# Kernel optimization log

Measured on AMD Instinct MI355X. Metric: run time of the kernel, lower is better.

## Reference

```python
import jax, jax.numpy as jnp
import numpy as np

P = 16; N_SIDE = 14; N_PATCH = 196
ENC_DIM = 1024; ENC_DEPTH = 2; ENC_HEADS = 16; ENC_DH = 64
DEC_DIM = 512; DEC_DEPTH = 1; DEC_HEADS = 8; DEC_DH = 64
NUM_MASKED = int(0.75 * N_PATCH)  # 147


def _ln(x, s, b):
    m = jnp.mean(x, axis=-1, keepdims=True)
    v = jnp.var(x, axis=-1, keepdims=True)
    return (x - m) * jax.lax.rsqrt(v + 1e-5) * s + b


def _mha(x, Wqkv, Wo, heads, dh):
    B, N, _ = x.shape
    q, k, v = jnp.split(x @ Wqkv, 3, axis=-1)
    rs = lambda t: t.reshape(B, N, heads, dh).transpose(0, 2, 1, 3)
    q, k, v = rs(q), rs(k), rs(v)
    scores = jnp.einsum('bhqd,bhkd->bhqk', q, k) / jnp.sqrt(jnp.float32(dh))
    att = jax.nn.softmax(scores, axis=-1)
    o = jnp.einsum('bhqk,bhkd->bhqd', att, v).transpose(0, 2, 1, 3).reshape(B, N, heads * dh)
    return o @ Wo


def _transformer(x, params, depth, heads, dh, lnfs, lnfb):
    (ln1s, ln1b, Wqkv, Wo, ln2s, ln2b, W1, b1, W2, b2) = params
    for i in range(depth):
        x = x + _mha(_ln(x, ln1s[i], ln1b[i]), Wqkv[i], Wo[i], heads, dh)
        h = jax.nn.gelu(_ln(x, ln2s[i], ln2b[i]) @ W1[i] + b1[i])
        x = x + h @ W2[i] + b2[i]
    return _ln(x, lnfs, lnfb)


def setup_inputs() -> dict:
    key = jax.random.key(0)
    ks = jax.random.split(key, 24)
    B = 64
    w = lambda k, s: (jax.random.normal(k, s, jnp.float32) * 0.02)
    E, IE = ENC_DIM, ENC_HEADS * ENC_DH
    D, ID = DEC_DIM, DEC_HEADS * DEC_DH
    d = {}
    d['images'] = jax.random.normal(ks[0], (B, 224, 224, 3), jnp.float32)
    d['rand'] = jax.random.uniform(ks[1], (B, N_PATCH), dtype=jnp.float32)
    d['patch_W'] = w(ks[2], (P * P * 3, E)); d['patch_b'] = jnp.zeros((E,), jnp.float32)
    d['pos_emb'] = w(ks[3], (N_PATCH, E))
    d['enc_ln1s'] = jnp.ones((ENC_DEPTH, E), jnp.float32); d['enc_ln1b'] = jnp.zeros((ENC_DEPTH, E), jnp.float32)
    d['enc_Wqkv'] = w(ks[4], (ENC_DEPTH, E, 3 * IE)); d['enc_Wo'] = w(ks[5], (ENC_DEPTH, IE, E))
    d['enc_ln2s'] = jnp.ones((ENC_DEPTH, E), jnp.float32); d['enc_ln2b'] = jnp.zeros((ENC_DEPTH, E), jnp.float32)
    d['enc_W1'] = w(ks[6], (ENC_DEPTH, E, 4 * E)); d['enc_b1'] = jnp.zeros((ENC_DEPTH, 4 * E), jnp.float32)
    d['enc_W2'] = w(ks[7], (ENC_DEPTH, 4 * E, E)); d['enc_b2'] = jnp.zeros((ENC_DEPTH, E), jnp.float32)
    d['enc_lnfs'] = jnp.ones((E,), jnp.float32); d['enc_lnfb'] = jnp.zeros((E,), jnp.float32)
    d['e2d_W'] = w(ks[8], (E, D)); d['e2d_b'] = jnp.zeros((D,), jnp.float32)
    d['mask_token'] = w(ks[9], (D,))
    d['dec_pos'] = w(ks[10], (N_PATCH, D))
    d['dec_ln1s'] = jnp.ones((DEC_DEPTH, D), jnp.float32); d['dec_ln1b'] = jnp.zeros((DEC_DEPTH, D), jnp.float32)
    d['dec_Wqkv'] = w(ks[11], (DEC_DEPTH, D, 3 * ID)); d['dec_Wo'] = w(ks[12], (DEC_DEPTH, ID, D))
    d['dec_ln2s'] = jnp.ones((DEC_DEPTH, D), jnp.float32); d['dec_ln2b'] = jnp.zeros((DEC_DEPTH, D), jnp.float32)
    d['dec_W1'] = w(ks[13], (DEC_DEPTH, D, 4 * D)); d['dec_b1'] = jnp.zeros((DEC_DEPTH, 4 * D), jnp.float32)
    d['dec_W2'] = w(ks[14], (DEC_DEPTH, 4 * D, D)); d['dec_b2'] = jnp.zeros((DEC_DEPTH, D), jnp.float32)
    d['dec_lnfs'] = jnp.ones((D,), jnp.float32); d['dec_lnfb'] = jnp.zeros((D,), jnp.float32)
    d['pix_W'] = w(ks[15], (D, E)); d['pix_b'] = jnp.zeros((E,), jnp.float32)  # pixel_dim == encoder_dim per source
    return d


def reference(images, rand, patch_W, patch_b, pos_emb,
              enc_ln1s, enc_ln1b, enc_Wqkv, enc_Wo, enc_ln2s, enc_ln2b,
              enc_W1, enc_b1, enc_W2, enc_b2, enc_lnfs, enc_lnfb,
              e2d_W, e2d_b, mask_token, dec_pos,
              dec_ln1s, dec_ln1b, dec_Wqkv, dec_Wo, dec_ln2s, dec_ln2b,
              dec_W1, dec_b1, dec_W2, dec_b2, dec_lnfs, dec_lnfb,
              pix_W, pix_b):
    B = images.shape[0]
    # patch embed: [B,224,224,3] -> [B,196,768] -> [B,196,1024]
    x = images.reshape(B, N_SIDE, P, N_SIDE, P, 3).transpose(0, 1, 3, 2, 4, 5).reshape(B, N_PATCH, P * P * 3)
    patches = x @ patch_W + patch_b
    tokens = patches + pos_emb
    # random masking via argsort of uniform noise
    order = jnp.argsort(rand, axis=-1)
    m_idx = order[:, :NUM_MASKED]        # [B,147]
    u_idx = order[:, NUM_MASKED:]        # [B,49]
    unmasked = jnp.take_along_axis(tokens, u_idx[:, :, None], axis=1)
    enc_params = (enc_ln1s, enc_ln1b, enc_Wqkv, enc_Wo, enc_ln2s, enc_ln2b, enc_W1, enc_b1, enc_W2, enc_b2)
    encoded = _transformer(unmasked, enc_params, ENC_DEPTH, ENC_HEADS, ENC_DH, enc_lnfs, enc_lnfb)
    dec_tok = encoded @ e2d_W + e2d_b + dec_pos[u_idx]
    mask_toks = mask_token + dec_pos[m_idx]
    bidx = jnp.arange(B)[:, None]
    all_tok = jnp.zeros((B, N_PATCH, DEC_DIM), dec_tok.dtype)
    all_tok = all_tok.at[bidx, u_idx].set(dec_tok)
    all_tok = all_tok.at[bidx, m_idx].set(mask_toks)
    dec_params = (dec_ln1s, dec_ln1b, dec_Wqkv, dec_Wo, dec_ln2s, dec_ln2b, dec_W1, dec_b1, dec_W2, dec_b2)
    decoded = _transformer(all_tok, dec_params, DEC_DEPTH, DEC_HEADS, DEC_DH, dec_lnfs, dec_lnfb)
    pred = jnp.take_along_axis(decoded, m_idx[:, :, None], axis=1) @ pix_W + pix_b
    target = jnp.take_along_axis(patches, m_idx[:, :, None], axis=1)
    return jnp.mean((pred - target) ** 2)
```

## Files before the change

kernel.cpp:

```cpp
#include <hip/hip_runtime.h>

typedef __attribute__((ext_vector_type(8))) __bf16 bf16x8;
typedef __attribute__((ext_vector_type(4))) float f32x4;

#define OFF_PATCH 0ull
#define OFF_X     25690112ull
#define OFF_LN    51380224ull
#define OFF_QKV   64225280ull
#define OFF_HID   103022592ull
#define OFF_WP    154402816ull
#define OFF_ORD   214695936ull
#define OFF_PART  214746112ull

#define WP_PATCH   0ull
#define WP_ENC_QKV 786432ull
#define WP_ENC_WO  7077888ull
#define WP_ENC_W1  9175040ull
#define WP_ENC_W2  17563648ull
#define WP_E2D     25952256ull
#define WP_DEC_QKV 26476544ull
#define WP_DEC_WO  27262976ull
#define WP_DEC_W1  27525120ull
#define WP_DEC_W2  28573696ull
#define WP_PIX     29622272ull

#define OM_BF16 0
#define OM_F32  1
#define OM_ACC  2
#define OM_GELU 3

__device__ __forceinline__ float b2f(unsigned short u) {
    return __uint_as_float(((unsigned int)u) << 16);
}
__device__ __forceinline__ unsigned short f2b(float f) {
    unsigned int x = __float_as_uint(f);
    x += 0x7fffu + ((x >> 16) & 1u);
    return (unsigned short)(x >> 16);
}
__device__ __forceinline__ float gelu_f(float x) {
    float u2 = 1.5957691216057308f * x * (1.f + 0.044715f * x * x);
    return x / (1.f + __expf(-u2));
}
__device__ __forceinline__ void gload16(const void* g, void* l) {
    __builtin_amdgcn_global_load_lds((const __attribute__((address_space(1))) void*)g,
                                     (__attribute__((address_space(3))) void*)l, 16, 0, 0);
}

__global__ __launch_bounds__(256) void pack_w(const float* __restrict__ in,
                                              unsigned short* __restrict__ out, int K, int N) {
    __shared__ float tile[32][33];
    int kt = blockIdx.y * 32, nt = blockIdx.x * 32;
    int tx = threadIdx.x & 31, ty = threadIdx.x >> 5;
#pragma unroll
    for (int i = 0; i < 32; i += 8) tile[ty + i][tx] = in[(size_t)(kt + ty + i) * N + nt + tx];
    __syncthreads();
#pragma unroll
    for (int i = 0; i < 32; i += 8)
        out[(size_t)(nt + ty + i) * K + kt + tx] = f2b(tile[tx][ty + i]);
}

__global__ __launch_bounds__(256) void patchify_kernel(const float* __restrict__ img,
                                                       unsigned short* __restrict__ Xp) {
    const long long total = 12544ll * 768;
    for (long long e = (long long)blockIdx.x * 256 + threadIdx.x; e < total;
         e += (long long)gridDim.x * 256) {
        int row = (int)(e / 768), k = (int)(e % 768);
        int b = row / 196, pi = row % 196;
        int py = pi / 14, px = pi % 14;
        int r = k / 48, rem = k % 48;
        int c = rem / 3, ch = rem % 3;
        long long src = (((long long)(b * 224 + py * 16 + r)) * 224 + (px * 16 + c)) * 3 + ch;
        Xp[e] = f2b(img[src]);
    }
}

template <int OM, bool ATOMIC>
__global__ __launch_bounds__(256) void gemm2(const unsigned short* __restrict__ A,
                                             const unsigned short* __restrict__ Bt,
                                             void* __restrict__ Cv,
                                             const float* __restrict__ bias,
                                             int M, int N, int K, int Kc) {
    __shared__ __align__(16) unsigned short As[2][128 * 64];
    __shared__ __align__(16) unsigned short Bs[2][128 * 64];
    const int tid = threadIdx.x, wave = tid >> 6, lane = tid & 63;
    int nwg = gridDim.x * gridDim.y;
    int orig = blockIdx.y * gridDim.x + blockIdx.x;
    int q = nwg >> 3, r8 = nwg & 7, xcd = orig & 7, off = orig >> 3;
    int wg = (xcd < r8 ? xcd * (q + 1) : r8 * (q + 1) + (xcd - r8) * q) + off;
    const int brow = (wg / gridDim.x) * 128, bcol = (wg % gridDim.x) * 128;
    const int kBeg = blockIdx.z * Kc;
    const int fr = lane & 15, fq = lane >> 4;
    const int wr = (wave >> 1) * 64, wc = (wave & 1) * 64;
    const int srow = wave * 32 + (lane >> 3);
    const int sca = ((lane & 7) ^ (lane >> 3)) * 8;
    const unsigned short* Ag = A + (size_t)(brow + srow) * K + kBeg + sca;
    const unsigned short* Bg = Bt + (size_t)(bcol + srow) * K + kBeg + sca;

    f32x4 acc[4][4];
#pragma unroll
    for (int m = 0; m < 4; ++m)
#pragma unroll
        for (int n = 0; n < 4; ++n) acc[m][n] = (f32x4){0.f, 0.f, 0.f, 0.f};

    auto stage = [&](int buf, int k0) {
        unsigned short* AsW = &As[buf][(wave * 32) * 64];
        unsigned short* BsW = &Bs[buf][(wave * 32) * 64];
#pragma unroll
        for (int i = 0; i < 4; ++i) {
            gload16(Ag + (size_t)(i * 8) * K + k0, AsW + i * 8 * 64);
            gload16(Bg + (size_t)(i * 8) * K + k0, BsW + i * 8 * 64);
        }
    };
    auto compute = [&](int buf) {
        const char* ab = (const char*)&As[buf][0];
        const char* bb = (const char*)&Bs[buf][0];
        const int sw = (fr & 7) << 4;
#pragma unroll
        for (int kk = 0; kk < 2; ++kk) {
            bf16x8 af[4], bf[4];
#pragma unroll
            for (int m = 0; m < 4; ++m)
                af[m] = *(const bf16x8*)(ab + (wr + m * 16 + fr) * 128 +
                                         ((kk * 64 + fq * 16) ^ sw));
#pragma unroll
            for (int n = 0; n < 4; ++n)
                bf[n] = *(const bf16x8*)(bb + (wc + n * 16 + fr) * 128 +
                                         ((kk * 64 + fq * 16) ^ sw));
#pragma unroll
            for (int m = 0; m < 4; ++m)
#pragma unroll
                for (int n = 0; n < 4; ++n)
                    acc[m][n] = __builtin_amdgcn_mfma_f32_16x16x32_bf16(af[m], bf[n],
                                                                       acc[m][n], 0, 0, 0);
        }
    };

    const int nt = Kc >> 6;
    stage(0, 0);
    __syncthreads();
    int cur = 0;
    for (int t = 0; t < nt - 1; ++t) {
        stage(cur ^ 1, (t + 1) << 6);
        compute(cur);
        __syncthreads();
        cur ^= 1;
    }
    compute(cur);

    const bool addBias = (bias != nullptr) && (kBeg == 0);
#pragma unroll
    for (int m = 0; m < 4; ++m) {
        int rb = brow + wr + m * 16 + fq * 4;
#pragma unroll
        for (int r = 0; r < 4; ++r) {
            int row = rb + r;
            if (row < M) {
#pragma unroll
                for (int n = 0; n < 4; ++n) {
                    int col = bcol + wc + n * 16 + fr;
                    float v = acc[m][n][r];
                    if (addBias) v += bias[col];
                    size_t o = (size_t)row * N + col;
                    if constexpr (ATOMIC) atomicAdd((float*)Cv + o, v);
                    else if constexpr (OM == OM_BF16) ((unsigned short*)Cv)[o] = f2b(v);
                    else if constexpr (OM == OM_F32) ((float*)Cv)[o] = v;
                    else if constexpr (OM == OM_ACC) ((float*)Cv)[o] += v;
                    else ((unsigned short*)Cv)[o] = f2b(gelu_f(v));
                }
            }
        }
    }
}

template <int N, int H, int NW>
__global__ __launch_bounds__(NW * 64) void attn_mfma(const unsigned short* __restrict__ qkv,
                                                     unsigned short* __restrict__ out) {
    constexpr int Npad = ((N + 31) / 32) * 32;
    constexpr int NT = Npad / 16;
    constexpr int KS = Npad / 32;
    constexpr int PS = Npad + 8;
    constexpr int SQ = 3 * H * 64, SO = H * 64;
    __shared__ __align__(16) unsigned short Kl[Npad * 64];
    __shared__ __align__(16) unsigned short Vt[64 * PS];
    __shared__ __align__(16) unsigned short Pl[NW * 16 * PS];
    const int b = blockIdx.x / H, h = blockIdx.x % H;
    const unsigned short* base = qkv + (size_t)b * N * SQ;
    const int qoff = h * 64, koff = (H + h) * 64, voff = (2 * H + h) * 64;
    const int tid = threadIdx.x, wave = tid >> 6, lane = tid & 63;
    const int fr = lane & 15, fq = lane >> 4;

    for (int idx = tid; idx < Npad * 8; idx += NW * 64) {
        int row = idx >> 3, ch = idx & 7;
        uint4 v = {0u, 0u, 0u, 0u};
        if (row < N) v = *(const uint4*)(base + (size_t)row * SQ + koff + ch * 8);
        *(uint4*)((char*)Kl + row * 128 + ((ch * 16) ^ ((row & 7) << 4))) = v;
    }
    for (int idx = tid; idx < Npad * 32; idx += NW * 64) {
        int key = idx >> 5, d2 = (idx & 31) * 2;
        unsigned int v = 0;
        if (key < N) v = *(const unsigned int*)(base + (size_t)key * SQ + voff + d2);
        Vt[d2 * PS + key] = (unsigned short)(v & 0xffffu);
        Vt[(d2 + 1) * PS + key] = (unsigned short)(v >> 16);
    }
    __syncthreads();

    unsigned short* pw = Pl + wave * 16 * PS;
    for (int qt = wave; qt < NT; qt += NW) {
        const int q0 = qt * 16;
        int qr = q0 + fr;
        if (qr > N - 1) qr = N - 1;
        const unsigned short* qp = base + (size_t)qr * SQ + qoff + fq * 8;
        bf16x8 aq0 = *(const bf16x8*)qp;
        bf16x8 aq1 = *(const bf16x8*)(qp + 32);
        f32x4 sa[NT];
#pragma unroll
        for (int ct = 0; ct < NT; ++ct) sa[ct] = (f32x4){0.f, 0.f, 0.f, 0.f};
#pragma unroll
        for (int ct = 0; ct < NT; ++ct) {
            const char* kb = (const char*)Kl + (ct * 16 + fr) * 128;
            bf16x8 kf0 = *(const bf16x8*)(kb + ((fq * 16) ^ ((fr & 7) << 4)));
            bf16x8 kf1 = *(const bf16x8*)(kb + ((64 + fq * 16) ^ ((fr & 7) << 4)));
            sa[ct] = __builtin_amdgcn_mfma_f32_16x16x32_bf16(aq0, kf0, sa[ct], 0, 0, 0);
            sa[ct] = __builtin_amdgcn_mfma_f32_16x16x32_bf16(aq1, kf1, sa[ct], 0, 0, 0);
        }
        float mrow[4] = {-3e38f, -3e38f, -3e38f, -3e38f};
#pragma unroll
        for (int ct = 0; ct < NT; ++ct) {
            bool ok = (ct * 16 + fr) < N;
#pragma unroll
            for (int r = 0; r < 4; ++r) {
                float s = ok ? sa[ct][r] * 0.125f : -3e38f;
                sa[ct][r] = s;
                mrow[r] = fmaxf(mrow[r], s);
            }
        }
#pragma unroll
        for (int off = 1; off <= 8; off <<= 1)
#pragma unroll
            for (int r = 0; r < 4; ++r) mrow[r] = fmaxf(mrow[r], __shfl_xor(mrow[r], off));
        float ssum[4] = {0.f, 0.f, 0.f, 0.f};
#pragma unroll
        for (int ct = 0; ct < NT; ++ct)
#pragma unroll
            for (int r = 0; r < 4; ++r) {
                float p = __expf(sa[ct][r] - mrow[r]);
                sa[ct][r] = p;
                ssum[r] += p;
            }
#pragma unroll
        for (int off = 1; off <= 8; off <<= 1)
#pragma unroll
            for (int r = 0; r < 4; ++r) ssum[r] += __shfl_xor(ssum[r], off);
#pragma unroll
        for (int ct = 0; ct < NT; ++ct)
#pragma unroll
            for (int r = 0; r < 4; ++r)
                pw[(fq * 4 + r) * PS + ct * 16 + fr] = f2b(sa[ct][r]);
        f32x4 oa[4];
#pragma unroll
        for (int vt = 0; vt < 4; ++vt) oa[vt] = (f32x4){0.f, 0.f, 0.f, 0.f};
#pragma unroll
        for (int ks = 0; ks < KS; ++ks) {
            bf16x8 pa = *(const bf16x8*)(pw + fr * PS + ks * 32 + fq * 8);
#pragma unroll
            for (int vt = 0; vt < 4; ++vt) {
                bf16x8 vf = *(const bf16x8*)(&Vt[(vt * 16 + fr) * PS + ks * 32 + fq * 8]);
                oa[vt] = __builtin_amdgcn_mfma_f32_16x16x32_bf16(pa, vf, oa[vt], 0, 0, 0);
            }
        }
        float inv[4];
#pragma unroll
        for (int r = 0; r < 4; ++r) inv[r] = 1.f / ssum[r];
#pragma unroll
        for (int vt = 0; vt < 4; ++vt)
#pragma unroll
            for (int r = 0; r < 4; ++r) {
                int q = q0 + fq * 4 + r;
                if (q < N)
                    out[((size_t)b * N + q) * SO + h * 64 + vt * 16 + fr] =
                        f2b(oa[vt][r] * inv[r]);
            }
    }
}

__global__ __launch_bounds__(256) void argsort_kernel(const float* __restrict__ rnd,
                                                      int* __restrict__ ord) {
    __shared__ float vals[196];
    int b = blockIdx.x, t = threadIdx.x;
    if (t < 196) vals[t] = rnd[b * 196 + t];
    __syncthreads();
    if (t < 196) {
        float v = vals[t];
        int rank = 0;
        for (int j = 0; j < 196; ++j) {
            float vj = vals[j];
            rank += (vj < v) || (vj == v && j < t);
        }
        ord[b * 196 + rank] = t;
    }
}

__global__ __launch_bounds__(256) void gather_unmasked(const unsigned short* __restrict__ patches,
                                                       const float* __restrict__ pos,
                                                       const int* __restrict__ ord,
                                                       float* __restrict__ xe) {
    int row = blockIdx.x;
    int b = row / 49, i = row % 49;
    int src = ord[b * 196 + 147 + i];
    const unsigned short* pr = patches + ((size_t)(b * 196 + src) << 10);
    const float* pe = pos + ((size_t)src << 10);
    float* o = xe + ((size_t)row << 10);
    int d = threadIdx.x * 4;
    ushort4 pv = *(const ushort4*)(pr + d);
    float4 p4 = *(const float4*)(pe + d);
    float4 r;
    r.x = b2f(pv.x) + p4.x; r.y = b2f(pv.y) + p4.y;
    r.z = b2f(pv.z) + p4.z; r.w = b2f(pv.w) + p4.w;
    *(float4*)(o + d) = r;
}

template <int L>
__global__ __launch_bounds__(256) void ln_kernel(const float* __restrict__ x,
                                                 unsigned short* __restrict__ y,
                                                 const float* __restrict__ sw,
                                                 const float* __restrict__ bw) {
    __shared__ float red[8];
    const int tid = threadIdx.x;
    const float* xr = x + (size_t)blockIdx.x * L;
    float sum = 0.f, sq = 0.f;
    for (int i = tid * 4; i < L; i += 1024) {
        float4 v = *(const float4*)(xr + i);
        sum += v.x + v.y + v.z + v.w;
        sq += v.x * v.x + v.y * v.y + v.z * v.z + v.w * v.w;
    }
    for (int off = 32; off; off >>= 1) {
        sum += __shfl_xor(sum, off);
        sq += __shfl_xor(sq, off);
    }
    int wave = tid >> 6, lane = tid & 63;
    if (lane == 0) { red[wave] = sum; red[4 + wave] = sq; }
    __syncthreads();
    float ts = red[0] + red[1] + red[2] + red[3];
    float tq = red[4] + red[5] + red[6] + red[7];
    float mean = ts / L;
    float inv = rsqrtf(tq / L - mean * mean + 1e-5f);
    unsigned short* yr = y + (size_t)blockIdx.x * L;
    for (int i = tid * 4; i < L; i += 1024) {
        float4 v = *(const float4*)(xr + i);
        float4 s4 = *(const float4*)(sw + i);
        float4 b4 = *(const float4*)(bw + i);
        ushort4 o;
        o.x = f2b((v.x - mean) * inv * s4.x + b4.x);
        o.y = f2b((v.y - mean) * inv * s4.y + b4.y);
        o.z = f2b((v.z - mean) * inv * s4.z + b4.z);
        o.w = f2b((v.w - mean) * inv * s4.w + b4.w);
        *(ushort4*)(yr + i) = o;
    }
}

__global__ __launch_bounds__(256) void scatter_tokens(const float* __restrict__ dec_tok,
                                                      const float* __restrict__ dec_pos,
                                                      const float* __restrict__ mask_tok,
                                                      const int* __restrict__ ord,
                                                      float* __restrict__ all_tok) {
    int e = blockIdx.x;
    int b = e / 196, i = e % 196;
    int idx = ord[e];
    float* o = all_tok + ((size_t)(b * 196 + idx)) * 512;
    const float* dp = dec_pos + (size_t)idx * 512;
    int d = threadIdx.x * 4;
    if (d < 512) {
        float4 dv = *(const float4*)(dp + d);
        float4 sv;
        if (i < 147) sv = *(const float4*)(mask_tok + d);
        else sv = *(const float4*)(dec_tok + ((size_t)(b * 49 + (i - 147))) * 512 + d);
        float4 r = {sv.x + dv.x, sv.y + dv.y, sv.z + dv.z, sv.w + dv.w};
        *(float4*)(o + d) = r;
    }
}

__global__ __launch_bounds__(256) void gather_masked(const unsigned short* __restrict__ x,
                                                     const int* __restrict__ ord,
                                                     unsigned short* __restrict__ gm) {
    int r = blockIdx.x;
    int b = r / 147, j = r % 147;
    int idx = ord[b * 196 + j];
    const unsigned short* src = x + ((size_t)(b * 196 + idx)) * 512;
    unsigned short* o = gm + (size_t)r * 512;
    int d = threadIdx.x * 4;
    if (d < 512) *(ushort4*)(o + d) = *(const ushort4*)(src + d);
}

__global__ __launch_bounds__(256) void loss_partial(const float* __restrict__ pred,
                                                    const unsigned short* __restrict__ patches,
                                                    const int* __restrict__ ord,
                                                    float* __restrict__ part) {
    __shared__ float red[8];
    float local = 0.f;
    const long long total = 9633792ll;
    for (long long e = (long long)blockIdx.x * 256 + threadIdx.x; e < total; e += 4096ll * 256) {
        int r = (int)(e >> 10), d = (int)(e & 1023);
        int b = r / 147, j = r % 147;
        int idx = ord[b * 196 + j];
        float t = b2f(patches[(((size_t)(b * 196 + idx)) << 10) + d]);
        float df = pred[e] - t;
        local += df * df;
    }
    for (int off = 32; off; off >>= 1) local += __shfl_xor(local, off);
    int wave = threadIdx.x >> 6, lane = threadIdx.x & 63;
    if (lane == 0) red[wave] = local;
    __syncthreads();
    if (threadIdx.x == 0) part[blockIdx.x] = red[0] + red[1] + red[2] + red[3];
}

__global__ __launch_bounds__(256) void loss_final(const float* __restrict__ part,
                                                  float* __restrict__ out) {
    __shared__ float red[8];
    float local = 0.f;
    for (int i = threadIdx.x; i < 4096; i += 256) local += part[i];
    for (int off = 32; off; off >>= 1) local += __shfl_xor(local, off);
    int wave = threadIdx.x >> 6, lane = threadIdx.x & 63;
    if (lane == 0) red[wave] = local;
    __syncthreads();
    if (threadIdx.x == 0) out[0] = (red[0] + red[1] + red[2] + red[3]) / 9633792.0f;
}

extern "C" void kernel_launch(void* const* d_in, const int* in_sizes, int n_in, void* d_out,
                              int out_size, void* d_ws, size_t ws_size, hipStream_t stream) {
    const float* images = (const float*)d_in[0];
    const float* rnd = (const float*)d_in[1];
    const float* patch_W = (const float*)d_in[2];
    const float* patch_b = (const float*)d_in[3];
    const float* pos_emb = (const float*)d_in[4];
    const float* enc_ln1s = (const float*)d_in[5];
    const float* enc_ln1b = (const float*)d_in[6];
    const float* enc_Wqkv = (const float*)d_in[7];
    const float* enc_Wo = (const float*)d_in[8];
    const float* enc_ln2s = (const float*)d_in[9];
    const float* enc_ln2b = (const float*)d_in[10];
    const float* enc_W1 = (const float*)d_in[11];
    const float* enc_b1 = (const float*)d_in[12];
    const float* enc_W2 = (const float*)d_in[13];
    const float* enc_b2 = (const float*)d_in[14];
    const float* enc_lnfs = (const float*)d_in[15];
    const float* enc_lnfb = (const float*)d_in[16];
    const float* e2d_W = (const float*)d_in[17];
    const float* e2d_b = (const float*)d_in[18];
    const float* mask_tok = (const float*)d_in[19];
    const float* dec_pos = (const float*)d_in[20];
    const float* dec_ln1s = (const float*)d_in[21];
    const float* dec_ln1b = (const float*)d_in[22];
    const float* dec_Wqkv = (const float*)d_in[23];
    const float* dec_Wo = (const float*)d_in[24];
    const float* dec_ln2s = (const float*)d_in[25];
    const float* dec_ln2b = (const float*)d_in[26];
    const float* dec_W1 = (const float*)d_in[27];
    const float* dec_b1 = (const float*)d_in[28];
    const float* dec_W2 = (const float*)d_in[29];
    const float* dec_b2 = (const float*)d_in[30];
    const float* dec_lnfs = (const float*)d_in[31];
    const float* dec_lnfb = (const float*)d_in[32];
    const float* pix_W = (const float*)d_in[33];
    const float* pix_b = (const float*)d_in[34];

    char* ws = (char*)d_ws;
    unsigned short* patches = (unsigned short*)(ws + OFF_PATCH);
    float* Rx = (float*)(ws + OFF_X);
    unsigned short* Rln = (unsigned short*)(ws + OFF_LN);
    unsigned short* RqkvB = (unsigned short*)(ws + OFF_QKV);
    float* RqkvF = (float*)(ws + OFF_QKV);
    unsigned short* Rhid = (unsigned short*)(ws + OFF_HID);
    unsigned short* wp = (unsigned short*)(ws + OFF_WP);
    int* ord = (int*)(ws + OFF_ORD);
    float* part = (float*)(ws + OFF_PART);
    float* out = (float*)d_out;

    auto PACK = [&](const float* src, size_t wpo, int K, int N) {
        pack_w<<<dim3(N / 32, K / 32), 256, 0, stream>>>(src, wp + wpo, K, N);
    };
    PACK(patch_W, WP_PATCH, 768, 1024);
    for (int l = 0; l < 2; ++l) {
        PACK(enc_Wqkv + (size_t)l * 1024 * 3072, WP_ENC_QKV + (size_t)l * 3145728, 1024, 3072);
        PACK(enc_Wo + (size_t)l * 1024 * 1024, WP_ENC_WO + (size_t)l * 1048576, 1024, 1024);
        PACK(enc_W1 + (size_t)l * 1024 * 4096, WP_ENC_W1 + (size_t)l * 4194304, 1024, 4096);
        PACK(enc_W2 + (size_t)l * 4096 * 1024, WP_ENC_W2 + (size_t)l * 4194304, 4096, 1024);
    }
    PACK(e2d_W, WP_E2D, 1024, 512);
    PACK(dec_Wqkv, WP_DEC_QKV, 512, 1536);
    PACK(dec_Wo, WP_DEC_WO, 512, 512);
    PACK(dec_W1, WP_DEC_W1, 512, 2048);
    PACK(dec_W2, WP_DEC_W2, 2048, 512);
    PACK(pix_W, WP_PIX, 512, 1024);

    auto GEMM = [&](int om, const unsigned short* A, size_t wpo, void* C, const float* bias,
                    int M, int N, int K, int S) {
        const unsigned short* Bt = wp + wpo;
        dim3 g(N / 128, (M + 127) / 128, S);
        int Kc = K / S;
        if (S > 1) {
            gemm2<OM_ACC, true><<<g, 256, 0, stream>>>(A, Bt, C, bias, M, N, K, Kc);
        } else if (om == OM_BF16) {
            gemm2<OM_BF16, false><<<g, 256, 0, stream>>>(A, Bt, C, bias, M, N, K, Kc);
        } else if (om == OM_F32) {
            gemm2<OM_F32, false><<<g, 256, 0, stream>>>(A, Bt, C, bias, M, N, K, Kc);
        } else if (om == OM_ACC) {
            gemm2<OM_ACC, false><<<g, 256, 0, stream>>>(A, Bt, C, bias, M, N, K, Kc);
        } else {
            gemm2<OM_GELU, false><<<g, 256, 0, stream>>>(A, Bt, C, bias, M, N, K, Kc);
        }
    };

    patchify_kernel<<<4096, 256, 0, stream>>>(images, Rhid);
    GEMM(OM_BF16, Rhid, WP_PATCH, patches, patch_b, 12544, 1024, 768, 1);
    argsort_kernel<<<64, 256, 0, stream>>>(rnd, ord);
    gather_unmasked<<<3136, 256, 0, stream>>>(patches, pos_emb, ord, Rx);

    for (int l = 0; l < 2; ++l) {
        ln_kernel<1024><<<3136, 256, 0, stream>>>(Rx, Rln, enc_ln1s + l * 1024,
                                                  enc_ln1b + l * 1024);
        GEMM(OM_BF16, Rln, WP_ENC_QKV + (size_t)l * 3145728, RqkvB, nullptr, 3136, 3072, 1024, 1);
        attn_mfma<49, 16, 4><<<64 * 16, 256, 0, stream>>>(RqkvB, Rhid);
        GEMM(OM_ACC, Rhid, WP_ENC_WO + (size_t)l * 1048576, Rx, nullptr, 3136, 1024, 1024, 2);
        ln_kernel<1024><<<3136, 256, 0, stream>>>(Rx, Rln, enc_ln2s + l * 1024,
                                                  enc_ln2b + l * 1024);
        GEMM(OM_GELU, Rln, WP_ENC_W1 + (size_t)l * 4194304, Rhid, enc_b1 + l * 4096, 3136,
             4096, 1024, 1);
        GEMM(OM_ACC, Rhid, WP_ENC_W2 + (size_t)l * 4194304, Rx, enc_b2 + l * 1024, 3136, 1024,
             4096, 4);
    }
    ln_kernel<1024><<<3136, 256, 0, stream>>>(Rx, Rln, enc_lnfs, enc_lnfb);

    GEMM(OM_F32, Rln, WP_E2D, RqkvF, e2d_b, 3136, 512, 1024, 1);
    scatter_tokens<<<12544, 256, 0, stream>>>(RqkvF, dec_pos, mask_tok, ord, Rx);

    ln_kernel<512><<<12544, 256, 0, stream>>>(Rx, Rln, dec_ln1s, dec_ln1b);
    GEMM(OM_BF16, Rln, WP_DEC_QKV, RqkvB, nullptr, 12544, 1536, 512, 1);
    attn_mfma<196, 8, 8><<<64 * 8, 512, 0, stream>>>(RqkvB, Rhid);
    GEMM(OM_ACC, Rhid, WP_DEC_WO, Rx, nullptr, 12544, 512, 512, 1);
    ln_kernel<512><<<12544, 256, 0, stream>>>(Rx, Rln, dec_ln2s, dec_ln2b);
    GEMM(OM_GELU, Rln, WP_DEC_W1, Rhid, dec_b1, 12544, 2048, 512, 1);
    GEMM(OM_ACC, Rhid, WP_DEC_W2, Rx, dec_b2, 12544, 512, 2048, 2);
    ln_kernel<512><<<12544, 256, 0, stream>>>(Rx, Rln, dec_lnfs, dec_lnfb);

    gather_masked<<<9408, 256, 0, stream>>>(Rln, ord, Rhid);
    GEMM(OM_F32, Rhid, WP_PIX, RqkvF, pix_b, 9408, 1024, 512, 1);
    loss_partial<<<4096, 256, 0, stream>>>(RqkvF, patches, ord, part);
    loss_final<<<1, 256, 0, stream>>>(part, out);
}
```

Measured before the change: 988.6 us.

## Switch GEMM from double-buffered to single-buffered LDS with precomputed swizzle offsets

The GEMM kernel drops its two-stage LDS double buffer and keeps a single 32 KB shared buffer. Each K-tile is loaded and then computed, with a barrier on both sides. LDS read addresses are precomputed once and combined with an XOR per k-subtile. Halving LDS use should allow more workgroups per CU and lower address arithmetic. The cost is that global loads for the next tile no longer overlap MFMA compute within a block.

```diff
diff --git a/kernel.cpp b/kernel.cpp
--- a/kernel.cpp
+++ b/kernel.cpp
@@ -80,8 +80,7 @@
                                              void* __restrict__ Cv,
                                              const float* __restrict__ bias,
                                              int M, int N, int K, int Kc) {
-    __shared__ __align__(16) unsigned short As[2][128 * 64];
-    __shared__ __align__(16) unsigned short Bs[2][128 * 64];
+    __shared__ __align__(16) unsigned short S[2 * 128 * 64];
     const int tid = threadIdx.x, wave = tid >> 6, lane = tid & 63;
     int nwg = gridDim.x * gridDim.y;
     int orig = blockIdx.y * gridDim.x + blockIdx.x;
@@ -95,6 +94,8 @@
     const int sca = ((lane & 7) ^ (lane >> 3)) * 8;
     const unsigned short* Ag = A + (size_t)(brow + srow) * K + kBeg + sca;
     const unsigned short* Bg = Bt + (size_t)(bcol + srow) * K + kBeg + sca;
+    unsigned short* AsW = S + wave * 32 * 64;
+    unsigned short* BsW = S + 128 * 64 + wave * 32 * 64;
 
     f32x4 acc[4][4];
 #pragma unroll
@@ -102,30 +103,31 @@
 #pragma unroll
         for (int n = 0; n < 4; ++n) acc[m][n] = (f32x4){0.f, 0.f, 0.f, 0.f};
 
-    auto stage = [&](int buf, int k0) {
-        unsigned short* AsW = &As[buf][(wave * 32) * 64];
-        unsigned short* BsW = &Bs[buf][(wave * 32) * 64];
+    const char* lds = (const char*)S;
+    const int sw = (fr & 7) << 4;
+    const int a0 = (wr + fr) * 128 + ((fq * 16) ^ sw);
+    const int b0 = 16384 + (wc + fr) * 128 + ((fq * 16) ^ sw);
+
+    const int nt = Kc >> 6;
+    for (int t = 0; t < nt; ++t) {
+        __syncthreads();
+        const int k0 = t << 6;
 #pragma unroll
         for (int i = 0; i < 4; ++i) {
             gload16(Ag + (size_t)(i * 8) * K + k0, AsW + i * 8 * 64);
             gload16(Bg + (size_t)(i * 8) * K + k0, BsW + i * 8 * 64);
         }
-    };
-    auto compute = [&](int buf) {
-        const char* ab = (const char*)&As[buf][0];
-        const char* bb = (const char*)&Bs[buf][0];
-        const int sw = (fr & 7) << 4;
+        __syncthreads();
 #pragma unroll
         for (int kk = 0; kk < 2; ++kk) {
+            const int kx = kk * 64;
             bf16x8 af[4], bf[4];
 #pragma unroll
             for (int m = 0; m < 4; ++m)
-                af[m] = *(const bf16x8*)(ab + (wr + m * 16 + fr) * 128 +
-                                         ((kk * 64 + fq * 16) ^ sw));
+                af[m] = *(const bf16x8*)(lds + ((a0 ^ kx) + m * 2048));
 #pragma unroll
             for (int n = 0; n < 4; ++n)
-                bf[n] = *(const bf16x8*)(bb + (wc + n * 16 + fr) * 128 +
-                                         ((kk * 64 + fq * 16) ^ sw));
+                bf[n] = *(const bf16x8*)(lds + ((b0 ^ kx) + n * 2048));
 #pragma unroll
             for (int m = 0; m < 4; ++m)
 #pragma unroll
@@ -133,19 +135,7 @@
                     acc[m][n] = __builtin_amdgcn_mfma_f32_16x16x32_bf16(af[m], bf[n],
                                                                        acc[m][n], 0, 0, 0);
         }
-    };
-
-    const int nt = Kc >> 6;
-    stage(0, 0);
-    __syncthreads();
-    int cur = 0;
-    for (int t = 0; t < nt - 1; ++t) {
-        stage(cur ^ 1, (t + 1) << 6);
-        compute(cur);
-        __syncthreads();
-        cur ^= 1;
-    }
-    compute(cur);
+    }
 
     const bool addBias = (bias != nullptr) && (kBeg == 0);
 #pragma unroll
```

Result: slower. 1.018 ms (+2.9%).
